# Optimization experiments

Measured on AMD Instinct MI355X. Metric: run time of the kernel, lower is better.

## Reference

```python
import jax, jax.numpy as jnp
import numpy as np

# geomloss SamplesLoss('sinkhorn', p=2, blur=0.05, scaling=0.5, debias=True) math
P = 2
BLUR = 0.05
SCALING = 0.5
DIAMETER = 64.0  # static conservative bound on point-cloud diameter for randn D=64 data


def _eps_schedule():
    eps_list = []
    e = DIAMETER ** P
    target = BLUR ** P
    while e > target:
        eps_list.append(e)
        e *= SCALING ** P
    eps_list.append(target)
    return np.array(eps_list, dtype=np.float32)


def _cost(x, y):
    # C_ij = ||x_i - y_j||^2 / 2   (p=2 cost of geomloss)
    sq = (jnp.sum(x * x, -1)[:, :, None] * 0.5
          + jnp.sum(y * y, -1)[:, None, :] * 0.5
          - jnp.einsum('bnd,bmd->bnm', x, y))
    return jnp.maximum(sq, 0.0)


def _softmin(eps, C, h):
    # f_i = -eps * log sum_j exp(h_j - C_ij / eps);  C: (B,N,M), h: (B,M)
    return -eps * jax.nn.logsumexp(h[:, None, :] - C / eps, axis=-1)


def setup_inputs() -> dict:
    key = jax.random.key(0)
    k1, k2, k3, k4 = jax.random.split(key, 4)
    B, N, M, D = 8, 2048, 2048, 64
    x = jax.random.normal(k1, (B, N, D), dtype=jnp.float32)
    y = jax.random.normal(k2, (B, M, D), dtype=jnp.float32)
    w1 = jax.random.uniform(k3, (B, N), dtype=jnp.float32) + 0.01
    w2 = jax.random.uniform(k4, (B, M), dtype=jnp.float32) + 0.01
    w1 = w1 / jnp.sum(w1, axis=-1, keepdims=True)
    w2 = w2 / jnp.sum(w2, axis=-1, keepdims=True)
    return {'x': x, 'y': y, 'w1': w1, 'w2': w2}


def _sinkhorn_divergence(x, y, w1, w2):
    a_log = jnp.log(w1)
    b_log = jnp.log(w2)
    eps_list = jnp.asarray(_eps_schedule())

    # --- Sinkhorn loop on detached quantities (geomloss detaches the loop) ---
    xd = jax.lax.stop_gradient(x)
    yd = jax.lax.stop_gradient(y)
    ald = jax.lax.stop_gradient(a_log)
    bld = jax.lax.stop_gradient(b_log)
    C_xy_d = _cost(xd, yd)
    C_yx_d = jnp.swapaxes(C_xy_d, 1, 2)
    C_xx_d = _cost(xd, xd)
    C_yy_d = _cost(yd, yd)

    eps0 = eps_list[0]
    f_ab = _softmin(eps0, C_xy_d, bld)
    g_ba = _softmin(eps0, C_yx_d, ald)
    f_aa = _softmin(eps0, C_xx_d, ald)
    g_bb = _softmin(eps0, C_yy_d, bld)

    def step(carry, eps):
        f_ab, g_ba, f_aa, g_bb = carry
        ft = _softmin(eps, C_xy_d, bld + g_ba / eps)
        gt = _softmin(eps, C_yx_d, ald + f_ab / eps)
        f_aa_t = _softmin(eps, C_xx_d, ald + f_aa / eps)
        g_bb_t = _softmin(eps, C_yy_d, bld + g_bb / eps)
        return (0.5 * (f_ab + ft), 0.5 * (g_ba + gt),
                0.5 * (f_aa + f_aa_t), 0.5 * (g_bb + g_bb_t)), None

    (f_ab, g_ba, f_aa, g_bb), _ = jax.lax.scan(step, (f_ab, g_ba, f_aa, g_bb), eps_list)

    # --- last extrapolation at eps = blur^p, differentiable ---
    eps = eps_list[-1]
    C_xy = _cost(x, y)
    C_yx = jnp.swapaxes(C_xy, 1, 2)
    C_xx = _cost(x, x)
    C_yy = _cost(y, y)
    f_ab_f = _softmin(eps, C_xy, b_log + g_ba / eps)
    g_ba_f = _softmin(eps, C_yx, a_log + f_ab / eps)
    f_aa_f = _softmin(eps, C_xx, a_log + f_aa / eps)
    g_bb_f = _softmin(eps, C_yy, b_log + g_bb / eps)

    # debiased sinkhorn cost per batch element
    loss = (jnp.sum(w1 * (f_ab_f - f_aa_f), axis=-1)
            + jnp.sum(w2 * (g_ba_f - g_bb_f), axis=-1))
    return loss


def reference(x, y, w1, w2):
    loss = _sinkhorn_divergence(x, y, w1, w2)
    return jnp.mean(loss)  # reduction='mean'
```

## Files before the change

### kernel.cpp

```cpp
#include <hip/hip_runtime.h>

#define NB 8
#define NN 2048
#define MM 2048
#define DD 64
#define NMAT ((size_t)NN * (size_t)MM)
#define NCHK 16
#define TS 128

#define CSCALE 320.0f
#define CDEC   (1.0f / CSCALE)

typedef _Float16 half_t;
typedef __attribute__((ext_vector_type(8))) _Float16 f16x8;
typedef __attribute__((ext_vector_type(4))) float f32x4;

__device__ unsigned short g_C[3 * NB * NMAT];
__device__ half_t g_xh[NB * NN * DD];
__device__ half_t g_yh[NB * MM * DD];
__device__ float g_fab[3][NB * NN], g_gba[3][NB * NN];
__device__ float g_faa[3][NB * NN], g_gbb[3][NB * NN];
__device__ float g_alog[NB * NN], g_blog[NB * NN];
__device__ float g_xn[NB * NN], g_yn[NB * NN];
__device__ float g_h0[NB * MM], g_h1[NB * NN], g_h2[NB * NN], g_h3[NB * MM];
__device__ float2 g_pfab[NB * NCHK * NN];
__device__ float2 g_pgba[NB * NCHK * NN];
__device__ float2 g_pfaa[NB * NCHK * NN];
__device__ float2 g_pgbb[NB * NCHK * NN];

__global__ __launch_bounds__(256) void prep_kernel(
    const float* __restrict__ x, const float* __restrict__ y,
    const float* __restrict__ w1, const float* __restrict__ w2)
{
  int gid = blockIdx.x * 256 + threadIdx.x;
  if (gid < NB * NN) {
    g_alog[gid] = logf(w1[gid]);
    g_blog[gid] = logf(w2[gid]);
  }
  int lane = threadIdx.x & 63;
  int row = blockIdx.x * 4 + (threadIdx.x >> 6);
  float xv = x[(size_t)row * DD + lane];
  float yv = y[(size_t)row * DD + lane];
  g_xh[(size_t)row * DD + lane] = (half_t)xv;
  g_yh[(size_t)row * DD + lane] = (half_t)yv;
  float sx = xv * xv;
  float sy = yv * yv;
#pragma unroll
  for (int off = 32; off > 0; off >>= 1) {
    sx += __shfl_down(sx, off);
    sy += __shfl_down(sy, off);
  }
  if (lane == 0) {
    g_xn[row] = 0.5f * sx;
    g_yn[row] = 0.5f * sy;
  }
}

__global__ __launch_bounds__(256) void cost_mfma()
{
  const int slab = blockIdx.z >> 3;
  const int b = blockIdx.z & 7;
  int I, J;
  if (slab) {
    if (blockIdx.x >= 136) return;
    int rem = blockIdx.x, ii = 0;
    while (rem >= NCHK - ii) { rem -= NCHK - ii; ++ii; }
    I = ii; J = ii + rem;
  } else {
    I = blockIdx.x >> 4;
    J = blockIdx.x & 15;
  }

  const half_t* Ah = (slab == 2) ? g_yh : g_xh;
  const half_t* Bh = (slab == 0) ? g_yh : ((slab == 1) ? g_xh : g_yh);
  const float* na = (slab == 2) ? g_yn : g_xn;
  const float* nbp = (slab == 0) ? g_yn : ((slab == 1) ? g_xn : g_yn);
  unsigned short* Cout = g_C + (size_t)slab * NB * NMAT + (size_t)b * NMAT;

  const int t = threadIdx.x;
  const int w = t >> 6, lane = t & 63;
  const int m = lane & 15, quad = lane >> 4;
  const int i0 = I * TS, j0 = J * TS;

  const half_t* Abase = Ah + ((size_t)b * NN + i0 + 32 * w + m) * DD + quad * 8;
  const half_t* Bbase = Bh + ((size_t)b * MM + j0 + m) * DD + quad * 8;

  f32x4 acc[2][8];
#pragma unroll
  for (int g = 0; g < 2; ++g)
#pragma unroll
    for (int c = 0; c < 8; ++c) acc[g][c] = (f32x4){0.f, 0.f, 0.f, 0.f};

#pragma unroll
  for (int s = 0; s < 2; ++s) {
    f16x8 a0 = *(const f16x8*)(Abase + s * 32);
    f16x8 a1 = *(const f16x8*)(Abase + (size_t)16 * DD + s * 32);
#pragma unroll
    for (int c = 0; c < 8; ++c) {
      f16x8 bf = *(const f16x8*)(Bbase + (size_t)(16 * c) * DD + s * 32);
      acc[0][c] = __builtin_amdgcn_mfma_f32_16x16x32_f16(a0, bf, acc[0][c], 0, 0, 0);
      acc[1][c] = __builtin_amdgcn_mfma_f32_16x16x32_f16(a1, bf, acc[1][c], 0, 0, 0);
    }
  }

  __shared__ unsigned short tile[TS * TS];
  float4 xr[2];
#pragma unroll
  for (int g = 0; g < 2; ++g)
    xr[g] = *(const float4*)(na + b * NN + i0 + 32 * w + 16 * g + 4 * quad);
#pragma unroll
  for (int c = 0; c < 8; ++c) {
    float yv = nbp[b * MM + j0 + 16 * c + m];
#pragma unroll
    for (int g = 0; g < 2; ++g) {
      float xg[4] = {xr[g].x, xr[g].y, xr[g].z, xr[g].w};
#pragma unroll
      for (int r = 0; r < 4; ++r) {
        float cv = fmaxf(xg[r] + yv - acc[g][c][r], 0.f);
        unsigned int u = __float2uint_rn(fminf(cv * CSCALE, 65535.f));
        tile[(32 * w + 16 * g + 4 * quad + r) * TS + 16 * c + m] = (unsigned short)u;
      }
    }
  }
  __syncthreads();

  const uint4* tl = (const uint4*)tile;
#pragma unroll
  for (int p = 0; p < 8; ++p) {
    int u = p * 256 + t;
    int row = u >> 4, c8 = (u & 15) * 8;
    *(uint4*)(Cout + (size_t)(i0 + row) * MM + j0 + c8) = tl[u];
  }
}

__global__ __launch_bounds__(256) void hprep_kernel(
    const float* __restrict__ fab_in, const float* __restrict__ gba_in,
    const float* __restrict__ faa_in, const float* __restrict__ gbb_in,
    float gs)
{
  int i = blockIdx.x * 256 + threadIdx.x;
  g_h0[i] = fmaf(gs, gba_in[i], g_blog[i]);
  g_h1[i] = fmaf(gs, fab_in[i], g_alog[i]);
  g_h2[i] = fmaf(gs, faa_in[i], g_alog[i]);
  g_h3[i] = fmaf(gs, gbb_in[i], g_blog[i]);
}

struct TileArgs {
  const unsigned short* C;
  const float* hrow;
  const float* hcol;
  float2* prow;
  float2* pcol;
  int sym;
};

__global__ __launch_bounds__(256) void tile_pass(
    TileArgs T0, TileArgs T1, TileArgs T2, float inv_eps)
{
  TileArgs A = (blockIdx.z == 0) ? T0 : (blockIdx.z == 1) ? T1 : T2;
  int I, J;
  if (A.sym) {
    if (blockIdx.x >= 136) return;
    int rem = blockIdx.x, ii = 0;
    while (rem >= NCHK - ii) { rem -= NCHK - ii; ++ii; }
    I = ii; J = ii + rem;
  } else {
    I = blockIdx.x >> 4;
    J = blockIdx.x & 15;
  }
  const int b = blockIdx.y;
  const int t = threadIdx.x;
  const int ctr = t & 15;
  const int rtr = t >> 4;
  const float csneg = -inv_eps * CDEC;

  const unsigned short* Cb = A.C + (size_t)b * NMAT
                           + (size_t)(I * TS) * MM + J * TS;

  float hr[8], hc[8];
  {
    const float* hrp = A.hrow + (size_t)b * MM + J * TS + ctr * 8;
    const float* hcp = A.hcol + (size_t)b * MM + I * TS + rtr * 8;
#pragma unroll
    for (int k = 0; k < 8; ++k) { hr[k] = hrp[k]; hc[k] = hcp[k]; }
  }

  uint4 cu[8];
#pragma unroll
  for (int r8 = 0; r8 < 8; ++r8)
    cu[r8] = *(const uint4*)(Cb + (size_t)(rtr * 8 + r8) * MM + ctr * 8);

  __shared__ float redR[TS][17], redC[TS][17];
  __shared__ float rowM[TS], colM[TS];

  float rm[8], cm[8];
#pragma unroll
  for (int k = 0; k < 8; ++k) { rm[k] = -3.0e38f; cm[k] = -3.0e38f; }
#pragma unroll
  for (int r8 = 0; r8 < 8; ++r8) {
    float base[8];
    base[0] = (float)(cu[r8].x & 0xffff) * csneg;
    base[1] = (float)(cu[r8].x >> 16)    * csneg;
    base[2] = (float)(cu[r8].y & 0xffff) * csneg;
    base[3] = (float)(cu[r8].y >> 16)    * csneg;
    base[4] = (float)(cu[r8].z & 0xffff) * csneg;
    base[5] = (float)(cu[r8].z >> 16)    * csneg;
    base[6] = (float)(cu[r8].w & 0xffff) * csneg;
    base[7] = (float)(cu[r8].w >> 16)    * csneg;
#pragma unroll
    for (int c8 = 0; c8 < 8; ++c8) {
      rm[r8] = fmaxf(rm[r8], hr[c8] + base[c8]);
      cm[c8] = fmaxf(cm[c8], hc[r8] + base[c8]);
    }
  }
#pragma unroll
  for (int r8 = 0; r8 < 8; ++r8) redR[rtr * 8 + r8][ctr] = rm[r8];
#pragma unroll
  for (int c8 = 0; c8 < 8; ++c8) redC[ctr * 8 + c8][rtr] = cm[c8];
  __syncthreads();
  if (t < TS) {
    float m = redR[t][0];
#pragma unroll
    for (int k = 1; k < 16; ++k) m = fmaxf(m, redR[t][k]);
    rowM[t] = m;
  } else {
    int tt = t - TS;
    float m = redC[tt][0];
#pragma unroll
    for (int k = 1; k < 16; ++k) m = fmaxf(m, redC[tt][k]);
    colM[tt] = m;
  }
  __syncthreads();

  float rmv[8], cmv[8];
#pragma unroll
  for (int k = 0; k < 8; ++k) {
    rmv[k] = rowM[rtr * 8 + k];
    cmv[k] = colM[ctr * 8 + k];
  }

  float rs[8], cs[8];
#pragma unroll
  for (int k = 0; k < 8; ++k) { rs[k] = 0.f; cs[k] = 0.f; }
#pragma unroll
  for (int r8 = 0; r8 < 8; ++r8) {
    float base[8];
    base[0] = (float)(cu[r8].x & 0xffff) * csneg;
    base[1] = (float)(cu[r8].x >> 16)    * csneg;
    base[2] = (float)(cu[r8].y & 0xffff) * csneg;
    base[3] = (float)(cu[r8].y >> 16)    * csneg;
    base[4] = (float)(cu[r8].z & 0xffff) * csneg;
    base[5] = (float)(cu[r8].z >> 16)    * csneg;
    base[6] = (float)(cu[r8].w & 0xffff) * csneg;
    base[7] = (float)(cu[r8].w >> 16)    * csneg;
#pragma unroll
    for (int c8 = 0; c8 < 8; ++c8) {
      rs[r8] += __expf(hr[c8] + base[c8] - rmv[r8]);
      cs[c8] += __expf(hc[r8] + base[c8] - cmv[c8]);
    }
  }
#pragma unroll
  for (int r8 = 0; r8 < 8; ++r8) redR[rtr * 8 + r8][ctr] = rs[r8];
#pragma unroll
  for (int c8 = 0; c8 < 8; ++c8) redC[ctr * 8 + c8][rtr] = cs[c8];
  __syncthreads();
  if (t < TS) {
    float s = 0.f;
#pragma unroll
    for (int k = 0; k < 16; ++k) s += redR[t][k];
    A.prow[((size_t)b * NCHK + J) * NN + I * TS + t] = make_float2(rowM[t], s);
  } else {
    int tt = t - TS;
    if (!(A.sym && I == J)) {
      float s = 0.f;
#pragma unroll
      for (int k = 0; k < 16; ++k) s += redC[tt][k];
      A.pcol[((size_t)b * NCHK + I) * NN + J * TS + tt] = make_float2(colM[tt], s);
    }
  }
}

struct MergeArgs {
  const float2* part;
  const float* fold;
  float* fout;
  const float* hbase;
  float* hout;
};

__global__ __launch_bounds__(256) void merge4(
    MergeArgs M0, MergeArgs M1, MergeArgs M2, MergeArgs M3,
    float eps, float alpha, float beta, float nextgs)
{
  MergeArgs A = (blockIdx.z == 0) ? M0 : (blockIdx.z == 1) ? M1
              : (blockIdx.z == 2) ? M2 : M3;
  const int b = blockIdx.y;
  const int i = blockIdx.x * 256 + threadIdx.x;
  float2 p[NCHK];
#pragma unroll
  for (int k = 0; k < NCHK; ++k)
    p[k] = A.part[((size_t)b * NCHK + k) * NN + i];
  float M = p[0].x;
#pragma unroll
  for (int k = 1; k < NCHK; ++k) M = fmaxf(M, p[k].x);
  float S = 0.f;
#pragma unroll
  for (int k = 0; k < NCHK; ++k) S += p[k].y * __expf(p[k].x - M);
  float ft = -eps * (M + __logf(S));
  int idx = b * NN + i;
  float fnew = alpha * A.fold[idx] + beta * ft;
  A.fout[idx] = fnew;
  A.hout[idx] = fmaf(nextgs, fnew, A.hbase[idx]);
}

__global__ __launch_bounds__(256) void loss_kernel(
    const float* __restrict__ w1, const float* __restrict__ w2,
    float* __restrict__ out)
{
  __shared__ float red[256];
  float acc = 0.f;
  for (int idx = threadIdx.x; idx < NB * NN; idx += 256) {
    acc += w1[idx] * (g_fab[2][idx] - g_faa[2][idx])
         + w2[idx] * (g_gba[2][idx] - g_gbb[2][idx]);
  }
  red[threadIdx.x] = acc;
  __syncthreads();
  for (int s = 128; s > 0; s >>= 1) {
    if (threadIdx.x < s) red[threadIdx.x] += red[threadIdx.x + s];
    __syncthreads();
  }
  if (threadIdx.x == 0) out[0] = red[0] * (1.0f / NB);
}

extern "C" void kernel_launch(void* const* d_in, const int* in_sizes, int n_in,
                              void* d_out, int out_size, void* d_ws, size_t ws_size,
                              hipStream_t stream)
{
  const float* x = (const float*)d_in[0];
  const float* y = (const float*)d_in[1];
  const float* w1 = (const float*)d_in[2];
  const float* w2 = (const float*)d_in[3];
  float* out = (float*)d_out;

  unsigned short* Cbase;
  hipGetSymbolAddress((void**)&Cbase, HIP_SYMBOL(g_C));
  unsigned short* Cxy = Cbase + 0ull * NB * NMAT;
  unsigned short* Cxx = Cbase + 1ull * NB * NMAT;
  unsigned short* Cyy = Cbase + 2ull * NB * NMAT;
  float *h0, *h1, *h2, *h3, *fabp, *gbap, *faap, *gbbp, *alog, *blog;
  float2 *pfab, *pgba, *pfaa, *pgbb;
  hipGetSymbolAddress((void**)&h0, HIP_SYMBOL(g_h0));
  hipGetSymbolAddress((void**)&h1, HIP_SYMBOL(g_h1));
  hipGetSymbolAddress((void**)&h2, HIP_SYMBOL(g_h2));
  hipGetSymbolAddress((void**)&h3, HIP_SYMBOL(g_h3));
  hipGetSymbolAddress((void**)&fabp, HIP_SYMBOL(g_fab));
  hipGetSymbolAddress((void**)&gbap, HIP_SYMBOL(g_gba));
  hipGetSymbolAddress((void**)&faap, HIP_SYMBOL(g_faa));
  hipGetSymbolAddress((void**)&gbbp, HIP_SYMBOL(g_gbb));
  hipGetSymbolAddress((void**)&alog, HIP_SYMBOL(g_alog));
  hipGetSymbolAddress((void**)&blog, HIP_SYMBOL(g_blog));
  hipGetSymbolAddress((void**)&pfab, HIP_SYMBOL(g_pfab));
  hipGetSymbolAddress((void**)&pgba, HIP_SYMBOL(g_pgba));
  hipGetSymbolAddress((void**)&pfaa, HIP_SYMBOL(g_pfaa));
  hipGetSymbolAddress((void**)&pgbb, HIP_SYMBOL(g_pgbb));

  auto fab = [&](int s) { return fabp + (size_t)s * NB * NN; };
  auto gba = [&](int s) { return gbap + (size_t)s * NB * NN; };
  auto faa = [&](int s) { return faap + (size_t)s * NB * NN; };
  auto gbb = [&](int s) { return gbbp + (size_t)s * NB * NN; };

  float eps_list[32];
  int ne = 0;
  {
    double v = 64.0 * 64.0;
    double tgt = 0.05 * 0.05;
    while (v > tgt) { eps_list[ne++] = (float)v; v *= 0.25; }
    eps_list[ne++] = (float)tgt;
  }

  prep_kernel<<<4096, 256, 0, stream>>>(x, y, w1, w2);

  cost_mfma<<<dim3(256, 1, 24), 256, 0, stream>>>();

  dim3 tg(256, NB, 3);
  dim3 mg(NN / 256, NB, 4);

  auto launch_iter = [&](float eps, float alpha, float beta, float nextgs,
                         int in, int outsel) {
    float inv = 1.0f / eps;
    TileArgs T0 = {Cxy, h0, h1, pfab, pgba, 0};
    TileArgs T1 = {Cxx, h2, h2, pfaa, pfaa, 1};
    TileArgs T2 = {Cyy, h3, h3, pgbb, pgbb, 1};
    tile_pass<<<tg, 256, 0, stream>>>(T0, T1, T2, inv);
    MergeArgs M0 = {pfab, fab(in), fab(outsel), alog, h1};
    MergeArgs M1 = {pgba, gba(in), gba(outsel), blog, h0};
    MergeArgs M2 = {pfaa, faa(in), faa(outsel), alog, h2};
    MergeArgs M3 = {pgbb, gbb(in), gbb(outsel), blog, h3};
    merge4<<<mg, 256, 0, stream>>>(M0, M1, M2, M3, eps, alpha, beta, nextgs);
  };

  hprep_kernel<<<64, 256, 0, stream>>>(fab(0), gba(0), faa(0), gbb(0), 0.f);
  launch_iter(eps_list[0], 0.f, 1.f, 1.0f / eps_list[0], 0, 0);

  int cur = 0;
  for (int k = 0; k < ne; ++k) {
    int nxt = 1 - cur;
    float nextgs = 1.0f / ((k < ne - 1) ? eps_list[k + 1] : eps_list[ne - 1]);
    launch_iter(eps_list[k], 0.5f, 0.5f, nextgs, cur, nxt);
    cur = nxt;
  }

  launch_iter(eps_list[ne - 1], 0.f, 1.f, 0.f, cur, 2);

  loss_kernel<<<1, 256, 0, stream>>>(w1, w2, out);
}
```

Baseline: 707.9 us.

## Recompute cost tiles with MFMA inside each Sinkhorn pass instead of storing them

Drops the precomputed 16-bit quantized cost matrices and recomputes each 128x128 cost tile on the fly with fp16 MFMA inside the per-iteration tile kernel, fusing the cost into the softmin. The aim is to remove the large per-iteration read of the stored cost matrices (hundreds of MB across the three slabs). The log-sum-exp is also moved to base 2 so it can use the hardware exp2 directly. The trade is extra MFMA and FMA work every iteration, and the cost now comes from fp16 inputs with fp32 accumulation instead of a 16-bit quantized value.

```diff
diff --git a/kernel.cpp b/kernel.cpp
--- a/kernel.cpp
+++ b/kernel.cpp
@@ -4,18 +4,15 @@
 #define NN 2048
 #define MM 2048
 #define DD 64
-#define NMAT ((size_t)NN * (size_t)MM)
 #define NCHK 16
 #define TS 128
-
-#define CSCALE 320.0f
-#define CDEC   (1.0f / CSCALE)
+#define L2E 1.4426950408889634f
+#define LN2 0.6931471805599453f
 
 typedef _Float16 half_t;
 typedef __attribute__((ext_vector_type(8))) _Float16 f16x8;
 typedef __attribute__((ext_vector_type(4))) float f32x4;
 
-__device__ unsigned short g_C[3 * NB * NMAT];
 __device__ half_t g_xh[NB * NN * DD];
 __device__ half_t g_yh[NB * MM * DD];
 __device__ float g_fab[3][NB * NN], g_gba[3][NB * NN];
@@ -34,8 +31,8 @@
 {
   int gid = blockIdx.x * 256 + threadIdx.x;
   if (gid < NB * NN) {
-    g_alog[gid] = logf(w1[gid]);
-    g_blog[gid] = logf(w2[gid]);
+    g_alog[gid] = log2f(w1[gid]);
+    g_blog[gid] = log2f(w2[gid]);
   }
   int lane = threadIdx.x & 63;
   int row = blockIdx.x * 4 + (threadIdx.x >> 6);
@@ -56,97 +53,23 @@
   }
 }
 
-__global__ __launch_bounds__(256) void cost_mfma()
-{
-  const int slab = blockIdx.z >> 3;
-  const int b = blockIdx.z & 7;
-  int I, J;
-  if (slab) {
-    if (blockIdx.x >= 136) return;
-    int rem = blockIdx.x, ii = 0;
-    while (rem >= NCHK - ii) { rem -= NCHK - ii; ++ii; }
-    I = ii; J = ii + rem;
-  } else {
-    I = blockIdx.x >> 4;
-    J = blockIdx.x & 15;
-  }
-
-  const half_t* Ah = (slab == 2) ? g_yh : g_xh;
-  const half_t* Bh = (slab == 0) ? g_yh : ((slab == 1) ? g_xh : g_yh);
-  const float* na = (slab == 2) ? g_yn : g_xn;
-  const float* nbp = (slab == 0) ? g_yn : ((slab == 1) ? g_xn : g_yn);
-  unsigned short* Cout = g_C + (size_t)slab * NB * NMAT + (size_t)b * NMAT;
-
-  const int t = threadIdx.x;
-  const int w = t >> 6, lane = t & 63;
-  const int m = lane & 15, quad = lane >> 4;
-  const int i0 = I * TS, j0 = J * TS;
-
-  const half_t* Abase = Ah + ((size_t)b * NN + i0 + 32 * w + m) * DD + quad * 8;
-  const half_t* Bbase = Bh + ((size_t)b * MM + j0 + m) * DD + quad * 8;
-
-  f32x4 acc[2][8];
-#pragma unroll
-  for (int g = 0; g < 2; ++g)
-#pragma unroll
-    for (int c = 0; c < 8; ++c) acc[g][c] = (f32x4){0.f, 0.f, 0.f, 0.f};
-
-#pragma unroll
-  for (int s = 0; s < 2; ++s) {
-    f16x8 a0 = *(const f16x8*)(Abase + s * 32);
-    f16x8 a1 = *(const f16x8*)(Abase + (size_t)16 * DD + s * 32);
-#pragma unroll
-    for (int c = 0; c < 8; ++c) {
-      f16x8 bf = *(const f16x8*)(Bbase + (size_t)(16 * c) * DD + s * 32);
-      acc[0][c] = __builtin_amdgcn_mfma_f32_16x16x32_f16(a0, bf, acc[0][c], 0, 0, 0);
-      acc[1][c] = __builtin_amdgcn_mfma_f32_16x16x32_f16(a1, bf, acc[1][c], 0, 0, 0);
-    }
-  }
-
-  __shared__ unsigned short tile[TS * TS];
-  float4 xr[2];
-#pragma unroll
-  for (int g = 0; g < 2; ++g)
-    xr[g] = *(const float4*)(na + b * NN + i0 + 32 * w + 16 * g + 4 * quad);
-#pragma unroll
-  for (int c = 0; c < 8; ++c) {
-    float yv = nbp[b * MM + j0 + 16 * c + m];
-#pragma unroll
-    for (int g = 0; g < 2; ++g) {
-      float xg[4] = {xr[g].x, xr[g].y, xr[g].z, xr[g].w};
-#pragma unroll
-      for (int r = 0; r < 4; ++r) {
-        float cv = fmaxf(xg[r] + yv - acc[g][c][r], 0.f);
-        unsigned int u = __float2uint_rn(fminf(cv * CSCALE, 65535.f));
-        tile[(32 * w + 16 * g + 4 * quad + r) * TS + 16 * c + m] = (unsigned short)u;
-      }
-    }
-  }
-  __syncthreads();
-
-  const uint4* tl = (const uint4*)tile;
-#pragma unroll
-  for (int p = 0; p < 8; ++p) {
-    int u = p * 256 + t;
-    int row = u >> 4, c8 = (u & 15) * 8;
-    *(uint4*)(Cout + (size_t)(i0 + row) * MM + j0 + c8) = tl[u];
-  }
-}
-
 __global__ __launch_bounds__(256) void hprep_kernel(
     const float* __restrict__ fab_in, const float* __restrict__ gba_in,
     const float* __restrict__ faa_in, const float* __restrict__ gbb_in,
-    float gs)
+    float gs2)
 {
   int i = blockIdx.x * 256 + threadIdx.x;
-  g_h0[i] = fmaf(gs, gba_in[i], g_blog[i]);
-  g_h1[i] = fmaf(gs, fab_in[i], g_alog[i]);
-  g_h2[i] = fmaf(gs, faa_in[i], g_alog[i]);
-  g_h3[i] = fmaf(gs, gbb_in[i], g_blog[i]);
-}
-
-struct TileArgs {
-  const unsigned short* C;
+  g_h0[i] = fmaf(gs2, gba_in[i], g_blog[i]);
+  g_h1[i] = fmaf(gs2, fab_in[i], g_alog[i]);
+  g_h2[i] = fmaf(gs2, faa_in[i], g_alog[i]);
+  g_h3[i] = fmaf(gs2, gbb_in[i], g_blog[i]);
+}
+
+struct FusedArgs {
+  const half_t* Af;
+  const half_t* Bf;
+  const float* nrow;
+  const float* ncol;
   const float* hrow;
   const float* hcol;
   float2* prow;
@@ -154,10 +77,10 @@
   int sym;
 };
 
-__global__ __launch_bounds__(256) void tile_pass(
-    TileArgs T0, TileArgs T1, TileArgs T2, float inv_eps)
-{
-  TileArgs A = (blockIdx.z == 0) ? T0 : (blockIdx.z == 1) ? T1 : T2;
+__global__ __launch_bounds__(256) void tile_fused(
+    FusedArgs T0, FusedArgs T1, FusedArgs T2, float keps)
+{
+  FusedArgs A = (blockIdx.z == 0) ? T0 : (blockIdx.z == 1) ? T1 : T2;
   int I, J;
   if (A.sym) {
     if (blockIdx.x >= 136) return;
@@ -170,112 +93,153 @@
   }
   const int b = blockIdx.y;
   const int t = threadIdx.x;
-  const int ctr = t & 15;
-  const int rtr = t >> 4;
-  const float csneg = -inv_eps * CDEC;
-
-  const unsigned short* Cb = A.C + (size_t)b * NMAT
-                           + (size_t)(I * TS) * MM + J * TS;
-
-  float hr[8], hc[8];
-  {
-    const float* hrp = A.hrow + (size_t)b * MM + J * TS + ctr * 8;
-    const float* hcp = A.hcol + (size_t)b * MM + I * TS + rtr * 8;
-#pragma unroll
-    for (int k = 0; k < 8; ++k) { hr[k] = hrp[k]; hc[k] = hcp[k]; }
-  }
-
-  uint4 cu[8];
-#pragma unroll
-  for (int r8 = 0; r8 < 8; ++r8)
-    cu[r8] = *(const uint4*)(Cb + (size_t)(rtr * 8 + r8) * MM + ctr * 8);
+  const int w = t >> 6, lane = t & 63;
+  const int m = lane & 15, quad = lane >> 4;
+  const int i0 = I * TS, j0 = J * TS;
+
+  const half_t* Abase = A.Af + ((size_t)b * NN + i0 + 32 * w + m) * DD + quad * 8;
+  const half_t* Bbase = A.Bf + ((size_t)b * MM + j0 + m) * DD + quad * 8;
+
+  f32x4 acc[2][8];
+#pragma unroll
+  for (int g = 0; g < 2; ++g)
+#pragma unroll
+    for (int c = 0; c < 8; ++c) acc[g][c] = (f32x4){0.f, 0.f, 0.f, 0.f};
+
+#pragma unroll
+  for (int s = 0; s < 2; ++s) {
+    f16x8 a0 = *(const f16x8*)(Abase + s * 32);
+    f16x8 a1 = *(const f16x8*)(Abase + (size_t)16 * DD + s * 32);
+#pragma unroll
+    for (int c = 0; c < 8; ++c) {
+      f16x8 bf = *(const f16x8*)(Bbase + (size_t)(16 * c) * DD + s * 32);
+      acc[0][c] = __builtin_amdgcn_mfma_f32_16x16x32_f16(a0, bf, acc[0][c], 0, 0, 0);
+      acc[1][c] = __builtin_amdgcn_mfma_f32_16x16x32_f16(a1, bf, acc[1][c], 0, 0, 0);
+    }
+  }
+
+  float4 xr[2], hq[2];
+#pragma unroll
+  for (int g = 0; g < 2; ++g) {
+    size_t ro = (size_t)b * NN + i0 + 32 * w + 16 * g + 4 * quad;
+    xr[g] = *(const float4*)(A.nrow + ro);
+    hq[g] = *(const float4*)(A.hcol + ro);
+  }
+  float ynk[8], hr[8];
+#pragma unroll
+  for (int c = 0; c < 8; ++c) {
+    size_t co = (size_t)b * MM + j0 + 16 * c + m;
+    ynk[c] = -A.ncol[co] * keps;
+    hr[c] = A.hrow[co];
+  }
+  float xnk[2][4], hcv[2][4];
+#pragma unroll
+  for (int g = 0; g < 2; ++g) {
+    xnk[g][0] = -xr[g].x * keps; xnk[g][1] = -xr[g].y * keps;
+    xnk[g][2] = -xr[g].z * keps; xnk[g][3] = -xr[g].w * keps;
+    hcv[g][0] = hq[g].x; hcv[g][1] = hq[g].y;
+    hcv[g][2] = hq[g].z; hcv[g][3] = hq[g].w;
+  }
+
+  float rm[2][4], cm[8];
+#pragma unroll
+  for (int g = 0; g < 2; ++g)
+#pragma unroll
+    for (int r = 0; r < 4; ++r) rm[g][r] = -3.0e38f;
+#pragma unroll
+  for (int c = 0; c < 8; ++c) cm[c] = -3.0e38f;
+
+#pragma unroll
+  for (int g = 0; g < 2; ++g)
+#pragma unroll
+    for (int c = 0; c < 8; ++c) {
+      f32x4 v = acc[g][c];
+#pragma unroll
+      for (int r = 0; r < 4; ++r) {
+        float bse = fminf(fmaf(v[r], keps, xnk[g][r]) + ynk[c], 0.f);
+        v[r] = bse;
+        rm[g][r] = fmaxf(rm[g][r], bse + hr[c]);
+        cm[c] = fmaxf(cm[c], bse + hcv[g][r]);
+      }
+      acc[g][c] = v;
+    }
 
   __shared__ float redR[TS][17], redC[TS][17];
   __shared__ float rowM[TS], colM[TS];
 
-  float rm[8], cm[8];
-#pragma unroll
-  for (int k = 0; k < 8; ++k) { rm[k] = -3.0e38f; cm[k] = -3.0e38f; }
-#pragma unroll
-  for (int r8 = 0; r8 < 8; ++r8) {
-    float base[8];
-    base[0] = (float)(cu[r8].x & 0xffff) * csneg;
-    base[1] = (float)(cu[r8].x >> 16)    * csneg;
-    base[2] = (float)(cu[r8].y & 0xffff) * csneg;
-    base[3] = (float)(cu[r8].y >> 16)    * csneg;
-    base[4] = (float)(cu[r8].z & 0xffff) * csneg;
-    base[5] = (float)(cu[r8].z >> 16)    * csneg;
-    base[6] = (float)(cu[r8].w & 0xffff) * csneg;
-    base[7] = (float)(cu[r8].w >> 16)    * csneg;
-#pragma unroll
-    for (int c8 = 0; c8 < 8; ++c8) {
-      rm[r8] = fmaxf(rm[r8], hr[c8] + base[c8]);
-      cm[c8] = fmaxf(cm[c8], hc[r8] + base[c8]);
-    }
-  }
-#pragma unroll
-  for (int r8 = 0; r8 < 8; ++r8) redR[rtr * 8 + r8][ctr] = rm[r8];
-#pragma unroll
-  for (int c8 = 0; c8 < 8; ++c8) redC[ctr * 8 + c8][rtr] = cm[c8];
+#pragma unroll
+  for (int g = 0; g < 2; ++g)
+#pragma unroll
+    for (int r = 0; r < 4; ++r)
+      redR[32 * w + 16 * g + 4 * quad + r][m] = rm[g][r];
+#pragma unroll
+  for (int c = 0; c < 8; ++c)
+    redC[16 * c + m][4 * w + quad] = cm[c];
   __syncthreads();
   if (t < TS) {
-    float m = redR[t][0];
-#pragma unroll
-    for (int k = 1; k < 16; ++k) m = fmaxf(m, redR[t][k]);
-    rowM[t] = m;
+    float mx = redR[t][0];
+#pragma unroll
+    for (int k = 1; k < 16; ++k) mx = fmaxf(mx, redR[t][k]);
+    rowM[t] = mx;
   } else {
     int tt = t - TS;
-    float m = redC[tt][0];
-#pragma unroll
-    for (int k = 1; k < 16; ++k) m = fmaxf(m, redC[tt][k]);
-    colM[tt] = m;
+    float mx = redC[tt][0];
+#pragma unroll
+    for (int k = 1; k < 16; ++k) mx = fmaxf(mx, redC[tt][k]);
+    colM[tt] = mx;
   }
   __syncthreads();
 
-  float rmv[8], cmv[8];
-#pragma unroll
-  for (int k = 0; k < 8; ++k) {
-    rmv[k] = rowM[rtr * 8 + k];
-    cmv[k] = colM[ctr * 8 + k];
-  }
-
-  float rs[8], cs[8];
-#pragma unroll
-  for (int k = 0; k < 8; ++k) { rs[k] = 0.f; cs[k] = 0.f; }
-#pragma unroll
-  for (int r8 = 0; r8 < 8; ++r8) {
-    float base[8];
-    base[0] = (float)(cu[r8].x & 0xffff) * csneg;
-    base[1] = (float)(cu[r8].x >> 16)    * csneg;
-    base[2] = (float)(cu[r8].y & 0xffff) * csneg;
-    base[3] = (float)(cu[r8].y >> 16)    * csneg;
-    base[4] = (float)(cu[r8].z & 0xffff) * csneg;
-    base[5] = (float)(cu[r8].z >> 16)    * csneg;
-    base[6] = (float)(cu[r8].w & 0xffff) * csneg;
-    base[7] = (float)(cu[r8].w >> 16)    * csneg;
-#pragma unroll
-    for (int c8 = 0; c8 < 8; ++c8) {
-      rs[r8] += __expf(hr[c8] + base[c8] - rmv[r8]);
-      cs[c8] += __expf(hc[r8] + base[c8] - cmv[c8]);
+  float rmv[2][4], cmv[8];
+#pragma unroll
+  for (int g = 0; g < 2; ++g) {
+    float4 q = *(const float4*)&rowM[32 * w + 16 * g + 4 * quad];
+    rmv[g][0] = q.x; rmv[g][1] = q.y; rmv[g][2] = q.z; rmv[g][3] = q.w;
+  }
+#pragma unroll
+  for (int c = 0; c < 8; ++c) cmv[c] = colM[16 * c + m];
+
+  float rs[2][4], cs[8];
+#pragma unroll
+  for (int g = 0; g < 2; ++g)
+#pragma unroll
+    for (int r = 0; r < 4; ++r) rs[g][r] = 0.f;
+#pragma unroll
+  for (int c = 0; c < 8; ++c) cs[c] = 0.f;
+
+#pragma unroll
+  for (int g = 0; g < 2; ++g)
+#pragma unroll
+    for (int c = 0; c < 8; ++c) {
+      f32x4 v = acc[g][c];
+#pragma unroll
+      for (int r = 0; r < 4; ++r) {
+        rs[g][r] += __builtin_amdgcn_exp2f(v[r] + hr[c] - rmv[g][r]);
+        cs[c] += __builtin_amdgcn_exp2f(v[r] + hcv[g][r] - cmv[c]);
+      }
     }
-  }
-#pragma unroll
-  for (int r8 = 0; r8 < 8; ++r8) redR[rtr * 8 + r8][ctr] = rs[r8];
-#pragma unroll
-  for (int c8 = 0; c8 < 8; ++c8) redC[ctr * 8 + c8][rtr] = cs[c8];
+
+#pragma unroll
+  for (int g = 0; g < 2; ++g)
+#pragma unroll
+    for (int r = 0; r < 4; ++r)
+      redR[32 * w + 16 * g + 4 * quad + r][m] = rs[g][r];
+#pragma unroll
+  for (int c = 0; c < 8; ++c)
+    redC[16 * c + m][4 * w + quad] = cs[c];
   __syncthreads();
   if (t < TS) {
     float s = 0.f;
 #pragma unroll
     for (int k = 0; k < 16; ++k) s += redR[t][k];
-    A.prow[((size_t)b * NCHK + J) * NN + I * TS + t] = make_float2(rowM[t], s);
+    A.prow[((size_t)b * NCHK + J) * NN + i0 + t] = make_float2(rowM[t], s);
   } else {
     int tt = t - TS;
     if (!(A.sym && I == J)) {
       float s = 0.f;
 #pragma unroll
       for (int k = 0; k < 16; ++k) s += redC[tt][k];
-      A.pcol[((size_t)b * NCHK + I) * NN + J * TS + tt] = make_float2(colM[tt], s);
+      A.pcol[((size_t)b * NCHK + I) * NN + j0 + tt] = make_float2(colM[tt], s);
     }
   }
 }
@@ -305,12 +269,12 @@
   for (int k = 1; k < NCHK; ++k) M = fmaxf(M, p[k].x);
   float S = 0.f;
 #pragma unroll
-  for (int k = 0; k < NCHK; ++k) S += p[k].y * __expf(p[k].x - M);
-  float ft = -eps * (M + __logf(S));
+  for (int k = 0; k < NCHK; ++k) S += p[k].y * __builtin_amdgcn_exp2f(p[k].x - M);
+  float ft = (-LN2 * eps) * (M + __log2f(S));
   int idx = b * NN + i;
   float fnew = alpha * A.fold[idx] + beta * ft;
   A.fout[idx] = fnew;
-  A.hout[idx] = fmaf(nextgs, fnew, A.hbase[idx]);
+  A.hout[idx] = fmaf(nextgs * L2E, fnew, A.hbase[idx]);
 }
 
 __global__ __launch_bounds__(256) void loss_kernel(
@@ -342,13 +306,14 @@
   const float* w2 = (const float*)d_in[3];
   float* out = (float*)d_out;
 
-  unsigned short* Cbase;
-  hipGetSymbolAddress((void**)&Cbase, HIP_SYMBOL(g_C));
-  unsigned short* Cxy = Cbase + 0ull * NB * NMAT;
-  unsigned short* Cxx = Cbase + 1ull * NB * NMAT;
-  unsigned short* Cyy = Cbase + 2ull * NB * NMAT;
+  half_t *xh, *yh;
+  float *xn, *yn;
   float *h0, *h1, *h2, *h3, *fabp, *gbap, *faap, *gbbp, *alog, *blog;
   float2 *pfab, *pgba, *pfaa, *pgbb;
+  hipGetSymbolAddress((void**)&xh, HIP_SYMBOL(g_xh));
+  hipGetSymbolAddress((void**)&yh, HIP_SYMBOL(g_yh));
+  hipGetSymbolAddress((void**)&xn, HIP_SYMBOL(g_xn));
+  hipGetSymbolAddress((void**)&yn, HIP_SYMBOL(g_yn));
   hipGetSymbolAddress((void**)&h0, HIP_SYMBOL(g_h0));
   hipGetSymbolAddress((void**)&h1, HIP_SYMBOL(g_h1));
   hipGetSymbolAddress((void**)&h2, HIP_SYMBOL(g_h2));
@@ -380,18 +345,16 @@
 
   prep_kernel<<<4096, 256, 0, stream>>>(x, y, w1, w2);
 
-  cost_mfma<<<dim3(256, 1, 24), 256, 0, stream>>>();
-
   dim3 tg(256, NB, 3);
   dim3 mg(NN / 256, NB, 4);
 
   auto launch_iter = [&](float eps, float alpha, float beta, float nextgs,
                          int in, int outsel) {
-    float inv = 1.0f / eps;
-    TileArgs T0 = {Cxy, h0, h1, pfab, pgba, 0};
-    TileArgs T1 = {Cxx, h2, h2, pfaa, pfaa, 1};
-    TileArgs T2 = {Cyy, h3, h3, pgbb, pgbb, 1};
-    tile_pass<<<tg, 256, 0, stream>>>(T0, T1, T2, inv);
+    float keps = L2E / eps;
+    FusedArgs T0 = {xh, yh, xn, yn, h0, h1, pfab, pgba, 0};
+    FusedArgs T1 = {xh, xh, xn, xn, h2, h2, pfaa, pfaa, 1};
+    FusedArgs T2 = {yh, yh, yn, yn, h3, h3, pgbb, pgbb, 1};
+    tile_fused<<<tg, 256, 0, stream>>>(T0, T1, T2, keps);
     MergeArgs M0 = {pfab, fab(in), fab(outsel), alog, h1};
     MergeArgs M1 = {pgba, gba(in), gba(outsel), blog, h0};
     MergeArgs M2 = {pfaa, faa(in), faa(outsel), alog, h2};
```

Result: slower. 1.070 ms (+51.2%).
